# Kernel tuning notes

Hardware: AMD Instinct MI355X
Metric: run time of the kernel (lower is better)

The kernel has to match this reference:

```python
import jax, jax.numpy as jnp
import numpy as np

WS = 7  # window size of the inner WindowAttention
EPS = 1e-5


def pc_roll(xb, shifts, axis):
    """Per-channel circular roll of [B,C,H,W] along `axis` (2 or 3).
    torch.roll semantics: out[i] = in[(i - shift) % n]."""
    n = xb.shape[axis]
    idx = (jnp.arange(n)[None, :] - shifts[:, None]) % n  # [C, n]
    if axis == 2:
        idxb = jnp.broadcast_to(idx[None, :, :, None], xb.shape)
    else:
        idxb = jnp.broadcast_to(idx[None, :, None, :], xb.shape)
    return jnp.take_along_axis(xb, idxb, axis=axis)


def layernorm(x, w, b):
    m = x.mean(-1, keepdims=True)
    v = x.var(-1, keepdims=True)
    return (x - m) * jax.lax.rsqrt(v + EPS) * w + b


def batchnorm2d(x, g, b):
    # training-mode BN: batch statistics over (B,H,W) per channel
    m = x.mean(axis=(0, 2, 3), keepdims=True)
    v = x.var(axis=(0, 2, 3), keepdims=True)
    return (x - m) * jax.lax.rsqrt(v + EPS) * g[None, :, None, None] + b[None, :, None, None]


def conv1x1(x, w, b):
    # x: [B,C,H,W], w: [Cout,Cin]
    return jnp.einsum('bchw,oc->bohw', x, w) + b[None, :, None, None]


def window_attention(q, k, v):
    # single-head Swin-style window attention, 7x7 windows, no rel-pos bias
    B, C, H, W = q.shape
    nh, nw = H // WS, W // WS

    def part(t):  # [B,C,H,W] -> [B*nh*nw, WS*WS, C]
        t = t.reshape(B, C, nh, WS, nw, WS)
        return t.transpose(0, 2, 4, 3, 5, 1).reshape(B * nh * nw, WS * WS, C)

    qw, kw, vw = part(q), part(k), part(v)
    scale = C ** -0.5
    attn = jax.nn.softmax(jnp.einsum('wnc,wmc->wnm', qw, kw) * scale, axis=-1)
    out = jnp.einsum('wnm,wmc->wnc', attn, vw)
    out = out.reshape(B, nh, nw, WS, WS, C).transpose(0, 5, 1, 3, 2, 4).reshape(B, C, H, W)
    return out


def setup_inputs() -> dict:
    B, H, W, C = 32, 56, 56, 128
    N = H * W
    key = jax.random.key(0)
    ks = jax.random.split(key, 16)
    f32 = jnp.float32

    def lin_w(k, din, dout):
        return 0.02 * jax.random.normal(k, (din, dout), dtype=f32)

    conv_std = float(np.sqrt(2.0 / C))
    inp = {
        'x': jax.random.normal(ks[0], (B, N, C), dtype=f32),
        'fc1_w': lin_w(ks[1], C, C), 'fc1_b': jnp.zeros((C,), f32),
        'fc2_w': lin_w(ks[2], C, C), 'fc2_b': jnp.zeros((C,), f32),
        'fc3_w': lin_w(ks[3], C, C), 'fc3_b': jnp.zeros((C,), f32),
        'fc4_w': lin_w(ks[4], C, C), 'fc4_b': jnp.zeros((C,), f32),
        'fc5_w': lin_w(ks[5], 2 * C, C), 'fc5_b': jnp.zeros((C,), f32),
        'fc6_w': lin_w(ks[6], 2 * C, C), 'fc6_b': jnp.zeros((C,), f32),
        'ln_w': jnp.ones((2 * C,), f32), 'ln_b': jnp.zeros((2 * C,), f32),
        'q_w': conv_std * jax.random.normal(ks[7], (C, C), dtype=f32), 'q_b': jnp.zeros((C,), f32),
        'k_w': conv_std * jax.random.normal(ks[8], (C, C), dtype=f32), 'k_b': jnp.zeros((C,), f32),
        'v_w': conv_std * jax.random.normal(ks[9], (C, C), dtype=f32), 'v_b': jnp.zeros((C,), f32),
        'bn1_g': jnp.ones((C,), f32), 'bn1_b': jnp.zeros((C,), f32),
        'bn2_g': jnp.ones((C,), f32), 'bn2_b': jnp.zeros((C,), f32),
        'H': H, 'W': W,
    }
    return inp


def reference(x, fc1_w, fc1_b, fc2_w, fc2_b, fc3_w, fc3_b, fc4_w, fc4_b,
              fc5_w, fc5_b, fc6_w, fc6_b, ln_w, ln_b,
              q_w, q_b, k_w, k_b, v_w, v_b, bn1_g, bn1_b, bn2_g, bn2_b, H, W):
    B, N, C = x.shape
    shifts = jnp.arange(C)
    gelu = lambda t: jax.nn.gelu(t, approximate=False)

    def to_bchw(t):
        return t.transpose(0, 2, 1).reshape(B, C, H, W)

    def to_bnc(t):
        return t.reshape(B, C, N).transpose(0, 2, 1)

    # branch 1: roll +c along H -> fc1 -> GELU -> roll +c along W -> fc2
    h = to_bnc(pc_roll(to_bchw(x), shifts, axis=2))
    h = gelu(h @ fc1_w + fc1_b)
    h = to_bnc(pc_roll(to_bchw(h), shifts, axis=3))
    x_1 = h @ fc2_w + fc2_b

    # branch 2: roll -c along W -> fc3 -> GELU -> roll +c along H -> fc4
    h = to_bnc(pc_roll(to_bchw(x), -shifts, axis=3))
    h = gelu(h @ fc3_w + fc3_b)
    h = to_bnc(pc_roll(to_bchw(h), shifts, axis=2))
    x_2 = h @ fc4_w + fc4_b

    x_1 = x_1 + x
    x_2 = x_2 + x
    x1 = jnp.concatenate([x_1, x_2], axis=2)          # [B,N,2C]
    x1 = layernorm(x1, ln_w, ln_b)
    x1 = x1 @ fc5_w + fc5_b
    x1 = x1 + x

    # local-attention branch (DWConv module actually runs WindowAtten + BN + ReLU)
    xb = to_bchw(x)
    att = window_attention(conv1x1(xb, q_w, q_b), conv1x1(xb, k_w, k_b), conv1x1(xb, v_w, v_b))
    x2 = jax.nn.relu(batchnorm2d(att, bn1_g, bn1_b))  # DWConv forward
    x2 = jax.nn.relu(x2)                              # act2 (idempotent, kept for fidelity)
    x2 = batchnorm2d(x2, bn2_g, bn2_b)                # norm2
    x2 = x2.reshape(B, C, N).transpose(0, 2, 1)       # [B,N,C]

    x3 = jnp.concatenate([x1, x2], axis=2)            # [B,N,2C]
    return x3 @ fc6_w + fc6_b
```

## Files before the change

### kernel.cpp

```cpp
#include <hip/hip_runtime.h>
#include <hip/hip_bf16.h>
#include <cstdint>
#include <cstddef>

typedef __bf16 bf16_t;
typedef __bf16 bf16x8 __attribute__((ext_vector_type(8)));
typedef float f32x4 __attribute__((ext_vector_type(4)));

#define B_SZ 32
#define H_SZ 56
#define W_SZ 56
#define N_TOK 3136
#define CH 128
#define M_TOT 100352

#define WOFF_FC1 0
#define WOFF_FC2 16384
#define WOFF_FC3 32768
#define WOFF_FC4 49152
#define WOFF_FC5 65536
#define WOFF_FC6 98304
#define WOFF_QW  131072
#define WOFF_KW  147456
#define WOFF_VW  163840
#define WTOT     180224

enum { A_FLAT = 0, A_WROLL, A_LN, A_BN };
enum { E_BIAS = 0, E_GELU, E_RES };

__device__ __forceinline__ float bf2f(bf16_t v) { return (float)v; }
__device__ __forceinline__ unsigned short bfbits(float v) {
    bf16_t b = (bf16_t)v; unsigned short u; __builtin_memcpy(&u, &b, 2); return u;
}

__global__ __launch_bounds__(256)
void wcvt_k(const float* __restrict__ f1, const float* __restrict__ f2,
            const float* __restrict__ f3, const float* __restrict__ f4,
            const float* __restrict__ f5, const float* __restrict__ f6,
            const float* __restrict__ qw, const float* __restrict__ kw,
            const float* __restrict__ vw, bf16_t* __restrict__ wb)
{
    const int blk = blockIdx.x;
    const int tid = threadIdx.x;
    if (blk < 32) {
        __shared__ bf16_t T[64][72];
        const float* src; bf16_t* dst; int K, t;
        if (blk < 4)       { src = f1; dst = wb + WOFF_FC1; K = 128; t = blk; }
        else if (blk < 8)  { src = f2; dst = wb + WOFF_FC2; K = 128; t = blk - 4; }
        else if (blk < 12) { src = f3; dst = wb + WOFF_FC3; K = 128; t = blk - 8; }
        else if (blk < 16) { src = f4; dst = wb + WOFF_FC4; K = 128; t = blk - 12; }
        else if (blk < 24) { src = f5; dst = wb + WOFF_FC5; K = 256; t = blk - 16; }
        else               { src = f6; dst = wb + WOFF_FC6; K = 256; t = blk - 24; }
        const int ti = t >> 1;
        const int tj = t & 1;
        for (int it = tid; it < 64 * 16; it += 256) {
            const int r = it >> 4, c4 = it & 15;
            float4 u = *(const float4*)(src + (size_t)(ti * 64 + r) * 128 + tj * 64 + c4 * 4);
            T[c4 * 4 + 0][r] = (bf16_t)u.x;
            T[c4 * 4 + 1][r] = (bf16_t)u.y;
            T[c4 * 4 + 2][r] = (bf16_t)u.z;
            T[c4 * 4 + 3][r] = (bf16_t)u.w;
        }
        __syncthreads();
        for (int it = tid; it < 64 * 8; it += 256) {
            const int n = it >> 3, ck = it & 7;
            *(uint4*)(dst + (size_t)(tj * 64 + n) * K + ti * 64 + ck * 8) =
                *(const uint4*)(&T[n][ck * 8]);
        }
    } else {
        const float* src; bf16_t* dst;
        int t = blk - 32;
        if (t < 4)      { src = qw; dst = wb + WOFF_QW; }
        else if (t < 8) { src = kw; dst = wb + WOFF_KW; t -= 4; }
        else            { src = vw; dst = wb + WOFF_VW; t -= 8; }
        const int base = t * 4096 + tid * 16;
        float4 u0 = *(const float4*)(src + base);
        float4 u1 = *(const float4*)(src + base + 4);
        float4 u2 = *(const float4*)(src + base + 8);
        float4 u3 = *(const float4*)(src + base + 12);
        bf16_t o[16] = {(bf16_t)u0.x, (bf16_t)u0.y, (bf16_t)u0.z, (bf16_t)u0.w,
                        (bf16_t)u1.x, (bf16_t)u1.y, (bf16_t)u1.z, (bf16_t)u1.w,
                        (bf16_t)u2.x, (bf16_t)u2.y, (bf16_t)u2.z, (bf16_t)u2.w,
                        (bf16_t)u3.x, (bf16_t)u3.y, (bf16_t)u3.z, (bf16_t)u3.w};
        *(uint4*)(dst + base) = *(const uint4*)o;
        *(uint4*)(dst + base + 8) = *(const uint4*)(o + 8);
    }
}

__global__ __launch_bounds__(256)
void transpose_k(const float* __restrict__ x, bf16_t* __restrict__ xT)
{
    __shared__ bf16_t T[128][70];
    const int tid = threadIdx.x;
    const int mbase = blockIdx.x * 64;
    const int bimg = mbase / N_TOK;
    const int n0 = mbase - bimg * N_TOK;
    for (int idx = tid; idx < 64 * 32; idx += 256) {
        const int tok = idx >> 5, cg = idx & 31;
        float4 u = *(const float4*)(x + (size_t)(mbase + tok) * CH + cg * 4);
        T[cg * 4 + 0][tok] = (bf16_t)u.x;
        T[cg * 4 + 1][tok] = (bf16_t)u.y;
        T[cg * 4 + 2][tok] = (bf16_t)u.z;
        T[cg * 4 + 3][tok] = (bf16_t)u.w;
    }
    __syncthreads();
    const uint* T32 = (const uint*)&T[0][0];
    for (int idx = tid; idx < 128 * 8; idx += 256) {
        const int c = idx >> 3, chunk = idx & 7;
        uint4 o;
        o.x = T32[c * 35 + chunk * 4 + 0];
        o.y = T32[c * 35 + chunk * 4 + 1];
        o.z = T32[c * 35 + chunk * 4 + 2];
        o.w = T32[c * 35 + chunk * 4 + 3];
        *(uint4*)(xT + ((size_t)(bimg * 128 + c)) * N_TOK + n0 + chunk * 8) = o;
    }
}

template<int AMODE, int KHALVES, int EPI, int WDIR, int OTRANS, int OF32>
__global__ __launch_bounds__(256)
void gemm_k(const bf16_t* __restrict__ A0, const bf16_t* __restrict__ A1,
            const bf16_t* __restrict__ Wt, const float* __restrict__ bias,
            const float* __restrict__ resid,
            const float* __restrict__ rowst,
            const float* __restrict__ lnw, const float* __restrict__ lnb,
            const float* __restrict__ bnp,
            void* __restrict__ outv)
{
    __shared__ __align__(16) char smem[17920];
    bf16_t* As = (bf16_t*)smem;
    const int tid = threadIdx.x;
    const int mbase = blockIdx.x * 64;
    const int bimg = mbase / N_TOK;
    const int n0 = mbase - bimg * N_TOK;
    const int lane = tid & 63;
    const int wv = tid >> 6;
    const int qd = lane >> 4;
    const int mr = lane & 15;
    const int KS = 128 * KHALVES;

    f32x4 acc[4][2];
#pragma unroll
    for (int i = 0; i < 4; ++i)
#pragma unroll
        for (int j = 0; j < 2; ++j) { f32x4 z = {0.f,0.f,0.f,0.f}; acc[i][j] = z; }

    for (int kh = 0; kh < KHALVES; ++kh) {
        if (kh) __syncthreads();
        if (AMODE == A_FLAT || AMODE == A_WROLL) {
            for (int idx = tid; idx < 128 * 8; idx += 256) {
                const int c = idx >> 3, chunk = idx & 7;
                const int cm = (c >= 112) ? c - 112 : (c >= 56 ? c - 56 : c);
                const bf16_t* crow = A0 + ((size_t)(bimg * 128 + c)) * N_TOK;
                if (AMODE == A_FLAT) {
                    int t = n0 + chunk * 8 + N_TOK - 56 * cm;
                    if (t >= N_TOK) t -= N_TOK;
                    uint4 u = *(const uint4*)(crow + t);
                    const bf16_t* up = (const bf16_t*)&u;
#pragma unroll
                    for (int j = 0; j < 8; ++j) As[(chunk * 8 + j) * 136 + c] = up[j];
                } else {
                    const int nl = n0 + chunk * 8;
                    const int h = nl / 56;
                    const int w0 = nl - h * 56;
                    int ws = (WDIR > 0) ? (w0 + cm) : (w0 + 56 - cm);
                    if (ws >= 56) ws -= 56;
                    const bf16_t* hrow = crow + h * 56;
                    if (ws <= 48) {
                        uint4 u = *(const uint4*)(hrow + ws);
                        const bf16_t* up = (const bf16_t*)&u;
#pragma unroll
                        for (int j = 0; j < 8; ++j) As[(chunk * 8 + j) * 136 + c] = up[j];
                    } else {
#pragma unroll
                        for (int j = 0; j < 8; ++j) {
                            int wj = ws + j; if (wj >= 56) wj -= 56;
                            As[(chunk * 8 + j) * 136 + c] = hrow[wj];
                        }
                    }
                }
            }
        } else if (AMODE == A_LN) {
            for (int idx = tid; idx < 64 * 16; idx += 256) {
                const int row = idx >> 4, ck = idx & 15;
                const int rowg = mbase + row;
                const bf16_t* src = kh ? A1 : A0;
                uint4 u = *(const uint4*)(src + (size_t)rowg * CH + ck * 8);
                const bf16_t* up = (const bf16_t*)&u;
                const float mean = rowst[2 * rowg];
                const float rstd = rowst[2 * rowg + 1];
                const int cabs = kh * 128 + ck * 8;
                bf16_t t[8];
#pragma unroll
                for (int j = 0; j < 8; ++j) {
                    float v = (bf2f(up[j]) - mean) * rstd;
                    v = v * lnw[cabs + j] + lnb[cabs + j];
                    t[j] = (bf16_t)v;
                }
                *(uint4*)(&As[row * 136 + ck * 8]) = *(const uint4*)t;
            }
        } else {
            for (int idx = tid; idx < 64 * 16; idx += 256) {
                const int row = idx >> 4, ck = idx & 15;
                const int rowg = mbase + row;
                if (kh == 0) {
                    uint4 u = *(const uint4*)(A0 + (size_t)rowg * CH + ck * 8);
                    *(uint4*)(&As[row * 136 + ck * 8]) = u;
                } else {
                    uint4 u = *(const uint4*)(A1 + (size_t)rowg * CH + ck * 8);
                    const bf16_t* up = (const bf16_t*)&u;
                    bf16_t t[8];
#pragma unroll
                    for (int j = 0; j < 8; ++j) {
                        const int c = ck * 8 + j;
                        float z = fmaxf(0.f, bf2f(up[j]) * bnp[c] + bnp[128 + c]);
                        t[j] = (bf16_t)(z * bnp[256 + c] + bnp[384 + c]);
                    }
                    *(uint4*)(&As[row * 136 + ck * 8]) = *(const uint4*)t;
                }
            }
        }
        __syncthreads();
        const bf16_t* wbase = Wt + (size_t)(wv * 32 + mr) * KS + kh * 128 + qd * 8;
#pragma unroll
        for (int kt = 0; kt < 4; ++kt) {
            bf16x8 af[4], bfr[2];
#pragma unroll
            for (int mt = 0; mt < 4; ++mt)
                af[mt] = *(const bf16x8*)(&As[(mt * 16 + mr) * 136 + kt * 32 + qd * 8]);
#pragma unroll
            for (int nt = 0; nt < 2; ++nt)
                bfr[nt] = *(const bf16x8*)(wbase + (size_t)(nt * 16) * KS + kt * 32);
#pragma unroll
            for (int mt = 0; mt < 4; ++mt)
#pragma unroll
                for (int nt = 0; nt < 2; ++nt)
                    acc[mt][nt] = __builtin_amdgcn_mfma_f32_16x16x32_bf16(
                        af[mt], bfr[nt], acc[mt][nt], 0, 0, 0);
        }
    }
    if (OTRANS) {
        __syncthreads();
        uint* T32 = (uint*)smem;
#pragma unroll
        for (int mt = 0; mt < 4; ++mt)
#pragma unroll
            for (int nt = 0; nt < 2; ++nt) {
                const int col = wv * 32 + nt * 16 + mr;
                const float bb = bias[col];
#pragma unroll
                for (int rp = 0; rp < 2; ++rp) {
                    float v0 = acc[mt][nt][2 * rp] + bb;
                    float v1 = acc[mt][nt][2 * rp + 1] + bb;
                    if (EPI == E_GELU) {
                        v0 = 0.5f * v0 * (1.f + erff(v0 * 0.70710678118654752f));
                        v1 = 0.5f * v1 * (1.f + erff(v1 * 0.70710678118654752f));
                    }
                    T32[col * 35 + mt * 8 + qd * 2 + rp] =
                        (uint)bfbits(v0) | ((uint)bfbits(v1) << 16);
                }
            }
        __syncthreads();
        const int c = tid >> 1, half = tid & 1;
        uint r[16];
#pragma unroll
        for (int j = 0; j < 16; ++j) r[j] = T32[c * 35 + half * 16 + j];
        bf16_t* op = (bf16_t*)outv + ((size_t)(bimg * 128 + c)) * N_TOK + n0 + half * 32;
        uint4 o0 = {r[0], r[1], r[2], r[3]};
        uint4 o1 = {r[4], r[5], r[6], r[7]};
        uint4 o2 = {r[8], r[9], r[10], r[11]};
        uint4 o3 = {r[12], r[13], r[14], r[15]};
        ((uint4*)op)[0] = o0; ((uint4*)op)[1] = o1;
        ((uint4*)op)[2] = o2; ((uint4*)op)[3] = o3;
    } else {
#pragma unroll
        for (int mt = 0; mt < 4; ++mt)
#pragma unroll
            for (int nt = 0; nt < 2; ++nt) {
                const int col = wv * 32 + nt * 16 + mr;
                const float bb = bias[col];
#pragma unroll
                for (int r = 0; r < 4; ++r) {
                    const int rowg = mbase + mt * 16 + qd * 4 + r;
                    float v = acc[mt][nt][r] + bb;
                    if (EPI == E_GELU) v = 0.5f * v * (1.f + erff(v * 0.70710678118654752f));
                    if (EPI == E_RES)  v += resid[(size_t)rowg * CH + col];
                    if (OF32) ((float*)outv)[(size_t)rowg * CH + col] = v;
                    else ((bf16_t*)outv)[(size_t)rowg * CH + col] = (bf16_t)v;
                }
            }
    }
}

__global__ __launch_bounds__(256)
void qkv_k(const float* __restrict__ x, const bf16_t* __restrict__ wb,
           const float* __restrict__ qb, const float* __restrict__ kb,
           const float* __restrict__ vb,
           bf16_t* __restrict__ qo, bf16_t* __restrict__ ko, bf16_t* __restrict__ vo)
{
    __shared__ __align__(16) bf16_t As[64 * 136];
    const int tid = threadIdx.x;
    const int mbase = blockIdx.x * 64;
    const int lane = tid & 63;
    const int wv = tid >> 6;
    const int qd = lane >> 4;
    const int mr = lane & 15;

    for (int idx = tid; idx < 64 * 16; idx += 256) {
        const int row = idx >> 4, ck = idx & 15;
        const float* p = x + (size_t)(mbase + row) * CH + ck * 8;
        float4 u0 = *(const float4*)p;
        float4 u1 = *(const float4*)(p + 4);
        bf16_t t[8] = {(bf16_t)u0.x, (bf16_t)u0.y, (bf16_t)u0.z, (bf16_t)u0.w,
                       (bf16_t)u1.x, (bf16_t)u1.y, (bf16_t)u1.z, (bf16_t)u1.w};
        *(uint4*)(&As[row * 136 + ck * 8]) = *(const uint4*)t;
    }
    __syncthreads();
    bf16x8 af[4][4];
#pragma unroll
    for (int kt = 0; kt < 4; ++kt)
#pragma unroll
        for (int mt = 0; mt < 4; ++mt)
            af[kt][mt] = *(const bf16x8*)(&As[(mt * 16 + mr) * 136 + kt * 32 + qd * 8]);

    const int woffs[3] = {WOFF_QW, WOFF_KW, WOFF_VW};
    const float* bs3[3] = {qb, kb, vb};
    bf16_t* os3[3] = {qo, ko, vo};
#pragma unroll
    for (int s = 0; s < 3; ++s) {
        const bf16_t* wbase = wb + woffs[s] + (size_t)(wv * 32 + mr) * 128 + qd * 8;
        f32x4 acc[4][2];
#pragma unroll
        for (int i = 0; i < 4; ++i)
#pragma unroll
            for (int j = 0; j < 2; ++j) { f32x4 z = {0.f,0.f,0.f,0.f}; acc[i][j] = z; }
#pragma unroll
        for (int kt = 0; kt < 4; ++kt) {
            bf16x8 bfr[2];
#pragma unroll
            for (int nt = 0; nt < 2; ++nt)
                bfr[nt] = *(const bf16x8*)(wbase + (nt * 16) * 128 + kt * 32);
#pragma unroll
            for (int mt = 0; mt < 4; ++mt)
#pragma unroll
                for (int nt = 0; nt < 2; ++nt)
                    acc[mt][nt] = __builtin_amdgcn_mfma_f32_16x16x32_bf16(
                        af[kt][mt], bfr[nt], acc[mt][nt], 0, 0, 0);
        }
        bf16_t* out = os3[s];
#pragma unroll
        for (int mt = 0; mt < 4; ++mt)
#pragma unroll
            for (int nt = 0; nt < 2; ++nt) {
                const int col = wv * 32 + nt * 16 + mr;
                const float bb = bs3[s][col];
#pragma unroll
                for (int r = 0; r < 4; ++r) {
                    const int rowg = mbase + mt * 16 + qd * 4 + r;
                    out[(size_t)rowg * CH + col] = (bf16_t)(acc[mt][nt][r] + bb);
                }
            }
    }
}

__global__ __launch_bounds__(256)
void rowstats_k(const bf16_t* __restrict__ x1p, const bf16_t* __restrict__ x2p,
                float* __restrict__ rs)
{
    const int row = blockIdx.x * 4 + (threadIdx.x >> 6);
    const int lane = threadIdx.x & 63;
    const bf16_t* p1 = x1p + (size_t)row * CH + lane * 2;
    const bf16_t* p2 = x2p + (size_t)row * CH + lane * 2;
    float a0 = bf2f(p1[0]), a1 = bf2f(p1[1]);
    float b0 = bf2f(p2[0]), b1 = bf2f(p2[1]);
    float s = a0 + a1 + b0 + b1;
    float sq = a0 * a0 + a1 * a1 + b0 * b0 + b1 * b1;
#pragma unroll
    for (int off = 32; off > 0; off >>= 1) {
        s += __shfl_down(s, off);
        sq += __shfl_down(sq, off);
    }
    if (lane == 0) {
        float mean = s * (1.f / 256.f);
        float var = sq * (1.f / 256.f) - mean * mean;
        rs[2 * row] = mean;
        rs[2 * row + 1] = rsqrtf(var + 1e-5f);
    }
}

__global__ __launch_bounds__(256, 4)
void attn_k(const bf16_t* __restrict__ qg, const bf16_t* __restrict__ kg,
            const bf16_t* __restrict__ vg, bf16_t* __restrict__ og,
            float* __restrict__ partial)
{
    __shared__ __align__(16) char smem[35840];
    bf16_t* Vr = (bf16_t*)smem;
    float*  Ss = (float*)smem;
    bf16_t* Ps = (bf16_t*)smem;
    bf16_t* Vt = (bf16_t*)(smem + 17408);
    bf16_t* Os = (bf16_t*)smem;
    float* bnacc = (float*)(smem + 34816);

    const int tid = threadIdx.x;
    const int blk = blockIdx.x;
    const int b = blk >> 6;
    const int wy = (blk >> 3) & 7;
    const int wx = blk & 7;
    const int lane = tid & 63;
    const int wv = tid >> 6;
    const int qd = lane >> 4;
    const int mr = lane & 15;

    bnacc[tid] = 0.f;

    for (int idx = tid; idx < 64 * 16; idx += 256) {
        const int i = idx >> 4, ck = idx & 15;
        uint4 uv = {0, 0, 0, 0};
        if (i < 49) {
            const int n = (wy * 7 + i / 7) * 56 + wx * 7 + (i % 7);
            uv = *(const uint4*)(vg + ((size_t)b * N_TOK + n) * CH + ck * 8);
        }
        *(uint4*)(&Vr[i * 136 + ck * 8]) = uv;
    }
    __syncthreads();

    const int vc = tid & 127, vhalf = tid >> 7;
    {
        uint4 vreg[4];
#pragma unroll
        for (int jc = 0; jc < 4; ++jc) {
            bf16_t t[8];
#pragma unroll
            for (int jj = 0; jj < 8; ++jj)
                t[jj] = Vr[(vhalf * 32 + jc * 8 + jj) * 136 + vc];
            vreg[jc] = *(const uint4*)t;
        }
#pragma unroll
        for (int jc = 0; jc < 4; ++jc)
            *(uint4*)(&Vt[vc * 68 + (vhalf * 4 + jc) * 8]) = vreg[jc];
    }
    __syncthreads();

    const int qrow = wv * 16 + mr;
    const int qc = qrow < 49 ? qrow : 48;
    const bf16_t* qptr = qg + ((size_t)b * N_TOK +
                               (wy * 7 + qc / 7) * 56 + wx * 7 + (qc % 7)) * CH + qd * 8;
    bf16x8 aq[4];
#pragma unroll
    for (int kt = 0; kt < 4; ++kt)
        aq[kt] = *(const bf16x8*)(qptr + kt * 32);

    f32x4 sacc[4];
#pragma unroll
    for (int nt = 0; nt < 4; ++nt) {
        const int krow = nt * 16 + mr;
        const int kc = krow < 49 ? krow : 48;
        const bf16_t* kptr = kg + ((size_t)b * N_TOK +
                                   (wy * 7 + kc / 7) * 56 + wx * 7 + (kc % 7)) * CH + qd * 8;
        f32x4 a = {0.f, 0.f, 0.f, 0.f};
#pragma unroll
        for (int kt = 0; kt < 4; ++kt) {
            bf16x8 bk = *(const bf16x8*)(kptr + kt * 32);
            a = __builtin_amdgcn_mfma_f32_16x16x32_bf16(aq[kt], bk, a, 0, 0, 0);
        }
        sacc[nt] = a;
    }
#pragma unroll
    for (int nt = 0; nt < 4; ++nt) {
        const int j = nt * 16 + mr;
#pragma unroll
        for (int r = 0; r < 4; ++r) {
            const int q = wv * 16 + qd * 4 + r;
            Ss[q * 68 + j] = (j < 49) ? sacc[nt][r] * 0.088388347648318447f : -1e30f;
        }
    }
    __syncthreads();

    {
        const int srow = tid >> 2, sq4 = tid & 3;
        const float* Sr = Ss + srow * 68 + sq4 * 16;
        float sv[16];
        *(float4*)(sv + 0)  = *(const float4*)(Sr + 0);
        *(float4*)(sv + 4)  = *(const float4*)(Sr + 4);
        *(float4*)(sv + 8)  = *(const float4*)(Sr + 8);
        *(float4*)(sv + 12) = *(const float4*)(Sr + 12);
        float mx = sv[0];
#pragma unroll
        for (int i = 1; i < 16; ++i) mx = fmaxf(mx, sv[i]);
        mx = fmaxf(mx, __shfl_xor(mx, 1));
        mx = fmaxf(mx, __shfl_xor(mx, 2));
        float sum = 0.f;
#pragma unroll
        for (int i = 0; i < 16; ++i) { sv[i] = __expf(sv[i] - mx); sum += sv[i]; }
        sum += __shfl_xor(sum, 1);
        sum += __shfl_xor(sum, 2);
        const float inv = 1.f / sum;
        __syncthreads();
        uint* P32 = (uint*)smem;
#pragma unroll
        for (int i = 0; i < 8; ++i) {
            const uint lo = bfbits(sv[2 * i] * inv);
            const uint hi = bfbits(sv[2 * i + 1] * inv);
            P32[srow * 36 + sq4 * 8 + i] = lo | (hi << 16);
        }
    }
    __syncthreads();

    bf16x8 ap[2];
    ap[0] = *(const bf16x8*)(&Ps[(wv * 16 + mr) * 72 + qd * 8]);
    ap[1] = *(const bf16x8*)(&Ps[(wv * 16 + mr) * 72 + 32 + qd * 8]);
    f32x4 oacc[8];
#pragma unroll
    for (int nt = 0; nt < 8; ++nt) {
        f32x4 a = {0.f, 0.f, 0.f, 0.f};
#pragma unroll
        for (int kt = 0; kt < 2; ++kt) {
            bf16x8 bv = *(const bf16x8*)(&Vt[(nt * 16 + mr) * 68 + kt * 32 + qd * 8]);
            a = __builtin_amdgcn_mfma_f32_16x16x32_bf16(ap[kt], bv, a, 0, 0, 0);
        }
        oacc[nt] = a;
    }

#pragma unroll
    for (int nt = 0; nt < 8; ++nt) {
        const int c = nt * 16 + mr;
        float s = 0.f, sq = 0.f;
#pragma unroll
        for (int r = 0; r < 4; ++r) {
            const int q = wv * 16 + qd * 4 + r;
            if (q < 49) { const float v = oacc[nt][r]; s += v; sq += v * v; }
        }
        s += __shfl_xor(s, 16); sq += __shfl_xor(sq, 16);
        s += __shfl_xor(s, 32); sq += __shfl_xor(sq, 32);
        if (qd == 0) { atomicAdd(&bnacc[c], s); atomicAdd(&bnacc[128 + c], sq); }
    }
    __syncthreads();

#pragma unroll
    for (int nt = 0; nt < 8; ++nt) {
        const int c = nt * 16 + mr;
#pragma unroll
        for (int r = 0; r < 4; ++r) {
            const int q = wv * 16 + qd * 4 + r;
            Os[q * 140 + c] = (bf16_t)oacc[nt][r];
        }
    }
    __syncthreads();

    for (int idx = tid; idx < 49 * 16; idx += 256) {
        const int row = idx >> 4, u = idx & 15;
        const int n = (wy * 7 + row / 7) * 56 + wx * 7 + (row % 7);
        *(uint4*)(og + ((size_t)b * N_TOK + n) * CH + u * 8) =
            *(const uint4*)(&Os[row * 140 + u * 8]);
    }
    partial[(size_t)blk * 256 + tid] = bnacc[tid];
}

__global__ __launch_bounds__(256)
void bnreduce_k(const float* __restrict__ partial, float* __restrict__ accum)
{
    const int t = threadIdx.x;
    const int r0 = blockIdx.x * 16;
    float s = 0.f;
#pragma unroll
    for (int r = 0; r < 16; ++r) s += partial[(size_t)(r0 + r) * 256 + t];
    atomicAdd(&accum[t], s);
}

__global__ __launch_bounds__(256)
void bnstats2_k(const bf16_t* __restrict__ att, const float* __restrict__ g1,
                const float* __restrict__ b1, float* __restrict__ accum)
{
    __shared__ float ls[256], lq[256];
    const int c = threadIdx.x & 127;
    const int half = threadIdx.x >> 7;
    const float m = accum[c] * (1.f / (float)M_TOT);
    const float var = accum[128 + c] * (1.f / (float)M_TOT) - m * m;
    const float rstd = rsqrtf(var + 1e-5f);
    const float scl = g1[c] * rstd;
    const float sh = b1[c] - m * scl;
    const size_t rowbase = (size_t)blockIdx.x * 196;
    float s = 0.f, sq = 0.f;
    for (int r = half; r < 196; r += 2) {
        float z = fmaxf(0.f, bf2f(att[(rowbase + r) * CH + c]) * scl + sh);
        s += z; sq += z * z;
    }
    ls[threadIdx.x] = s; lq[threadIdx.x] = sq;
    __syncthreads();
    if (threadIdx.x < 128) {
        atomicAdd(&accum[256 + c], ls[threadIdx.x] + ls[threadIdx.x + 128]);
        atomicAdd(&accum[384 + c], lq[threadIdx.x] + lq[threadIdx.x + 128]);
    }
}

__global__ void bnparams_k(const float* __restrict__ accum,
                           const float* __restrict__ g1, const float* __restrict__ b1,
                           const float* __restrict__ g2, const float* __restrict__ b2,
                           float* __restrict__ bnp)
{
    const int c = threadIdx.x;
    const float inv = 1.f / (float)M_TOT;
    float m1 = accum[c] * inv;
    float v1 = accum[128 + c] * inv - m1 * m1;
    float rs1 = rsqrtf(v1 + 1e-5f);
    float s1 = g1[c] * rs1;
    float sh1 = b1[c] - m1 * s1;
    float m2 = accum[256 + c] * inv;
    float v2 = accum[384 + c] * inv - m2 * m2;
    float rs2 = rsqrtf(v2 + 1e-5f);
    float s2 = g2[c] * rs2;
    float sh2 = b2[c] - m2 * s2;
    bnp[c] = s1; bnp[128 + c] = sh1; bnp[256 + c] = s2; bnp[384 + c] = sh2;
}

__global__ void zero_k(float* __restrict__ p) { p[threadIdx.x] = 0.f; }

extern "C" void kernel_launch(void* const* d_in, const int* in_sizes, int n_in,
                              void* d_out, int out_size, void* d_ws, size_t ws_size,
                              hipStream_t stream)
{
    (void)in_sizes; (void)n_in; (void)out_size; (void)ws_size;
    const float* x     = (const float*)d_in[0];
    const float* fc1_w = (const float*)d_in[1];
    const float* fc1_b = (const float*)d_in[2];
    const float* fc2_w = (const float*)d_in[3];
    const float* fc2_b = (const float*)d_in[4];
    const float* fc3_w = (const float*)d_in[5];
    const float* fc3_b = (const float*)d_in[6];
    const float* fc4_w = (const float*)d_in[7];
    const float* fc4_b = (const float*)d_in[8];
    const float* fc5_w = (const float*)d_in[9];
    const float* fc5_b = (const float*)d_in[10];
    const float* fc6_w = (const float*)d_in[11];
    const float* fc6_b = (const float*)d_in[12];
    const float* ln_w  = (const float*)d_in[13];
    const float* ln_b  = (const float*)d_in[14];
    const float* q_w   = (const float*)d_in[15];
    const float* q_b   = (const float*)d_in[16];
    const float* k_w   = (const float*)d_in[17];
    const float* k_b   = (const float*)d_in[18];
    const float* v_w   = (const float*)d_in[19];
    const float* v_b   = (const float*)d_in[20];
    const float* bn1_g = (const float*)d_in[21];
    const float* bn1_b = (const float*)d_in[22];
    const float* bn2_g = (const float*)d_in[23];
    const float* bn2_b = (const float*)d_in[24];

    char* ws = (char*)d_ws;
    const size_t SZB = (size_t)M_TOT * CH * sizeof(bf16_t);
    bf16_t* bufA = (bf16_t*)(ws);
    bf16_t* bufB = (bf16_t*)(ws + SZB);
    bf16_t* bufC = (bf16_t*)(ws + 2 * SZB);
    bf16_t* bufD = (bf16_t*)(ws + 3 * SZB);
    float*  rs   = (float*)(ws + 4 * SZB);
    float*  accum = (float*)(ws + 4 * SZB + (size_t)M_TOT * 2 * sizeof(float));
    float*  bnp  = accum + 512;
    float*  partial = bnp + 512;
    bf16_t* wbuf = (bf16_t*)(partial + 2048 * 256);

    const dim3 blk(256);
    const int GG = M_TOT / 64;

    zero_k<<<1, 512, 0, stream>>>(accum);
    wcvt_k<<<44, blk, 0, stream>>>(fc1_w, fc2_w, fc3_w, fc4_w, fc5_w, fc6_w,
                                   q_w, k_w, v_w, wbuf);
    transpose_k<<<GG, blk, 0, stream>>>(x, bufA);
    gemm_k<A_FLAT, 1, E_GELU, 0, 1, 0><<<GG, blk, 0, stream>>>(
        bufA, nullptr, wbuf + WOFF_FC1, fc1_b, nullptr, nullptr, nullptr, nullptr, nullptr, bufB);
    gemm_k<A_WROLL, 1, E_RES, -1, 0, 0><<<GG, blk, 0, stream>>>(
        bufB, nullptr, wbuf + WOFF_FC2, fc2_b, x, nullptr, nullptr, nullptr, nullptr, bufC);
    gemm_k<A_WROLL, 1, E_GELU, 1, 1, 0><<<GG, blk, 0, stream>>>(
        bufA, nullptr, wbuf + WOFF_FC3, fc3_b, nullptr, nullptr, nullptr, nullptr, nullptr, bufB);
    gemm_k<A_FLAT, 1, E_RES, 0, 0, 0><<<GG, blk, 0, stream>>>(
        bufB, nullptr, wbuf + WOFF_FC4, fc4_b, x, nullptr, nullptr, nullptr, nullptr, bufD);
    rowstats_k<<<M_TOT / 4, blk, 0, stream>>>(bufC, bufD, rs);
    gemm_k<A_LN, 2, E_RES, 0, 0, 0><<<GG, blk, 0, stream>>>(
        bufC, bufD, wbuf + WOFF_FC5, fc5_b, x, rs, ln_w, ln_b, nullptr, bufB);
    qkv_k<<<GG, blk, 0, stream>>>(x, wbuf, q_b, k_b, v_b, bufA, bufC, bufD);
    attn_k<<<B_SZ * 64, blk, 0, stream>>>(bufA, bufC, bufD, bufA, partial);
    bnreduce_k<<<128, blk, 0, stream>>>(partial, accum);
    bnstats2_k<<<512, blk, 0, stream>>>(bufA, bn1_g, bn1_b, accum);
    bnparams_k<<<1, 128, 0, stream>>>(accum, bn1_g, bn1_b, bn2_g, bn2_b, bnp);
    gemm_k<A_BN, 2, E_BIAS, 0, 0, 1><<<GG, blk, 0, stream>>>(
        bufB, bufA, wbuf + WOFF_FC6, fc6_b, nullptr, nullptr, nullptr, nullptr, bnp, d_out);
}
```

Before: 468.6 us.

## Compute softmax in registers and overlap V transpose with QK^T

Issues the V global loads into registers before the QK^T MFMAs so their latency is hidden behind the score computation. The V staging and transpose through shared memory now happen afterwards. Softmax is done directly on the MFMA accumulators using cross-lane shuffles, which removes the round trip of fp32 scores through shared memory and several barriers. The trade-off is higher register pressure from holding V in registers, and scattered 2-byte writes when storing P to shared memory.

```diff
diff --git a/kernel.cpp b/kernel.cpp
--- a/kernel.cpp
+++ b/kernel.cpp
@@ -394,7 +394,6 @@
 {
     __shared__ __align__(16) char smem[35840];
     bf16_t* Vr = (bf16_t*)smem;
-    float*  Ss = (float*)smem;
     bf16_t* Ps = (bf16_t*)smem;
     bf16_t* Vt = (bf16_t*)(smem + 17408);
     bf16_t* Os = (bf16_t*)smem;
@@ -412,33 +411,19 @@
 
     bnacc[tid] = 0.f;
 
-    for (int idx = tid; idx < 64 * 16; idx += 256) {
-        const int i = idx >> 4, ck = idx & 15;
+    const int vck = tid & 15;
+    const int vi0 = tid >> 4;
+    uint4 vld[4];
+#pragma unroll
+    for (int it = 0; it < 4; ++it) {
+        const int i = vi0 + it * 16;
         uint4 uv = {0, 0, 0, 0};
         if (i < 49) {
             const int n = (wy * 7 + i / 7) * 56 + wx * 7 + (i % 7);
-            uv = *(const uint4*)(vg + ((size_t)b * N_TOK + n) * CH + ck * 8);
-        }
-        *(uint4*)(&Vr[i * 136 + ck * 8]) = uv;
-    }
-    __syncthreads();
-
-    const int vc = tid & 127, vhalf = tid >> 7;
-    {
-        uint4 vreg[4];
-#pragma unroll
-        for (int jc = 0; jc < 4; ++jc) {
-            bf16_t t[8];
-#pragma unroll
-            for (int jj = 0; jj < 8; ++jj)
-                t[jj] = Vr[(vhalf * 32 + jc * 8 + jj) * 136 + vc];
-            vreg[jc] = *(const uint4*)t;
-        }
-#pragma unroll
-        for (int jc = 0; jc < 4; ++jc)
-            *(uint4*)(&Vt[vc * 68 + (vhalf * 4 + jc) * 8]) = vreg[jc];
-    }
-    __syncthreads();
+            uv = *(const uint4*)(vg + ((size_t)b * N_TOK + n) * CH + vck * 8);
+        }
+        vld[it] = uv;
+    }
 
     const int qrow = wv * 16 + mr;
     const int qc = qrow < 49 ? qrow : 48;
@@ -464,44 +449,60 @@
         }
         sacc[nt] = a;
     }
-#pragma unroll
-    for (int nt = 0; nt < 4; ++nt) {
-        const int j = nt * 16 + mr;
+
+#pragma unroll
+    for (int it = 0; it < 4; ++it)
+        *(uint4*)(&Vr[(vi0 + it * 16) * 136 + vck * 8]) = vld[it];
+    __syncthreads();
+
+    const int vc = tid & 127, vhalf = tid >> 7;
+    uint4 vreg[4];
+#pragma unroll
+    for (int jc = 0; jc < 4; ++jc) {
+        bf16_t t[8];
+#pragma unroll
+        for (int jj = 0; jj < 8; ++jj)
+            t[jj] = Vr[(vhalf * 32 + jc * 8 + jj) * 136 + vc];
+        vreg[jc] = *(const uint4*)t;
+    }
+    __syncthreads();
+
+#pragma unroll
+    for (int jc = 0; jc < 4; ++jc)
+        *(uint4*)(&Vt[vc * 68 + (vhalf * 4 + jc) * 8]) = vreg[jc];
+
+    {
+        const float SCALE = 0.088388347648318447f;
+#pragma unroll
+        for (int nt = 0; nt < 4; ++nt) {
+            const bool bad = (nt * 16 + mr) > 48;
+#pragma unroll
+            for (int r = 0; r < 4; ++r)
+                sacc[nt][r] = bad ? -1e30f : sacc[nt][r] * SCALE;
+        }
+        float pv[4][4];
+        float inv[4];
 #pragma unroll
         for (int r = 0; r < 4; ++r) {
-            const int q = wv * 16 + qd * 4 + r;
-            Ss[q * 68 + j] = (j < 49) ? sacc[nt][r] * 0.088388347648318447f : -1e30f;
-        }
-    }
-    __syncthreads();
-
-    {
-        const int srow = tid >> 2, sq4 = tid & 3;
-        const float* Sr = Ss + srow * 68 + sq4 * 16;
-        float sv[16];
-        *(float4*)(sv + 0)  = *(const float4*)(Sr + 0);
-        *(float4*)(sv + 4)  = *(const float4*)(Sr + 4);
-        *(float4*)(sv + 8)  = *(const float4*)(Sr + 8);
-        *(float4*)(sv + 12) = *(const float4*)(Sr + 12);
-        float mx = sv[0];
-#pragma unroll
-        for (int i = 1; i < 16; ++i) mx = fmaxf(mx, sv[i]);
-        mx = fmaxf(mx, __shfl_xor(mx, 1));
-        mx = fmaxf(mx, __shfl_xor(mx, 2));
-        float sum = 0.f;
-#pragma unroll
-        for (int i = 0; i < 16; ++i) { sv[i] = __expf(sv[i] - mx); sum += sv[i]; }
-        sum += __shfl_xor(sum, 1);
-        sum += __shfl_xor(sum, 2);
-        const float inv = 1.f / sum;
-        __syncthreads();
-        uint* P32 = (uint*)smem;
-#pragma unroll
-        for (int i = 0; i < 8; ++i) {
-            const uint lo = bfbits(sv[2 * i] * inv);
-            const uint hi = bfbits(sv[2 * i + 1] * inv);
-            P32[srow * 36 + sq4 * 8 + i] = lo | (hi << 16);
-        }
+            float m = fmaxf(fmaxf(sacc[0][r], sacc[1][r]), fmaxf(sacc[2][r], sacc[3][r]));
+            m = fmaxf(m, __shfl_xor(m, 1));
+            m = fmaxf(m, __shfl_xor(m, 2));
+            m = fmaxf(m, __shfl_xor(m, 4));
+            m = fmaxf(m, __shfl_xor(m, 8));
+#pragma unroll
+            for (int nt = 0; nt < 4; ++nt) pv[nt][r] = __expf(sacc[nt][r] - m);
+            float s = (pv[0][r] + pv[1][r]) + (pv[2][r] + pv[3][r]);
+            s += __shfl_xor(s, 1);
+            s += __shfl_xor(s, 2);
+            s += __shfl_xor(s, 4);
+            s += __shfl_xor(s, 8);
+            inv[r] = 1.f / s;
+        }
+#pragma unroll
+        for (int nt = 0; nt < 4; ++nt)
+#pragma unroll
+            for (int r = 0; r < 4; ++r)
+                Ps[(wv * 16 + qd * 4 + r) * 72 + nt * 16 + mr] = (bf16_t)(pv[nt][r] * inv[r]);
     }
     __syncthreads();
 
```

Result: no change. 463.2 us (-1.2%).
